# Optimization experiments

Measured on AMD Instinct MI355X. Metric: run time of the kernel, lower is better.

The kernel has to match this reference:

```python
import jax, jax.numpy as jnp
import numpy as np

EMB = 128  # embedding_size hard-coded in source
NW = 8192  # weak samples
NS = 8192  # strong samples
FD = 1024  # encoder input feature dim
QN = 1024  # queue max_size
C = 80     # num classes (COCO-style WSOD)


def setup_inputs() -> dict:
    key = jax.random.key(0)
    ks = jax.random.split(key, 9)
    return {
        "feats_strong": jax.random.normal(ks[0], (NS, FD), jnp.float32),
        "feats_weak": jax.random.normal(ks[1], (NW, FD), jnp.float32),
        "strong_labels": jax.random.randint(ks[2], (NS,), 0, C, jnp.int64),
        "weak_labels": jax.random.randint(ks[3], (NW,), 0, C, jnp.int64),
        "Wq": jax.random.normal(ks[4], (FD, EMB), jnp.float32) * (FD ** -0.5),
        "bq": jax.random.normal(ks[5], (EMB,), jnp.float32) * 0.01,
        "Wk": jax.random.normal(ks[6], (FD, EMB), jnp.float32) * (FD ** -0.5),
        "bk": jax.random.normal(ks[7], (EMB,), jnp.float32) * 0.01,
        "queue": jax.random.normal(ks[8], (QN, EMB), jnp.float32),
    }


def reference(feats_strong, feats_weak, strong_labels, weak_labels, Wq, bq, Wk, bk, queue):
    # Encoders applied to all samples at once (original loops one-by-one).
    q_all = feats_weak @ Wq + bq            # [NW, EMB]
    k_all = feats_strong @ Wk + bk          # [NS, EMB]
    k_all = jax.lax.stop_gradient(k_all)    # k = k.detach() in source

    w, s = weak_labels, strong_labels
    eq_ws = w[:, None] == s[None, :]                      # [NW, NS] weak-vs-strong label match
    cnt = eq_ws.astype(jnp.int32).sum(1)                  # num_strong per weak sample
    valid = cnt > 0                                       # `if weak_label in strong_labels`

    # rank of i among weak indices with the same label (position in torch.where output)
    eq_ww = (w[:, None] == w[None, :]).astype(jnp.int32)
    rank = jnp.tril(eq_ww, -1).sum(1)                     # [NW]
    sel = rank % jnp.maximum(cnt, 1)                      # `% num_strong`

    # occurrence rank of each strong index within its label group
    eq_ss = (s[:, None] == s[None, :]).astype(jnp.int32)
    occ = jnp.tril(eq_ss, -1).sum(1)                      # [NS]

    # index_strong[i] = sel[i]-th strong index whose label == w[i]
    M = eq_ws & (occ[None, :] == sel[:, None])            # [NW, NS]
    idx = jnp.argmax(M, axis=1)                           # [NW]

    q = q_all                                             # [NW, EMB]
    k = k_all[idx]                                        # [NW, EMB]

    l_pos = jnp.sum(q * k, axis=-1, keepdims=True)        # bmm([N,1,E],[N,E,1]) -> [N,1]
    l_neg = q @ queue.reshape(EMB, -1)                    # queue.view(EMB, -1): row-major reshape
    logits = jnp.concatenate([l_pos, l_neg], axis=1)      # [NW, 1+QN]

    # CrossEntropy with target 0 on each valid row, mean over valid rows
    ce = -jax.nn.log_softmax(logits, axis=-1)[:, 0]
    m = valid.astype(logits.dtype)
    loss = jnp.sum(ce * m) / jnp.maximum(m.sum(), 1.0)
    return loss
```

## Files before the change

kernel.cpp:

```cpp
#include <hip/hip_runtime.h>
#include <hip/hip_bf16.h>

#define NW   8192
#define NS   8192
#define FD   1024
#define EMB  128
#define QN   1024
#define NC   80

typedef unsigned short ushort_t;
typedef unsigned int   uint_t;
typedef __attribute__((ext_vector_type(8))) short short8;
typedef __attribute__((ext_vector_type(4))) float f32x4;

#define OFF_Q      0u
#define OFF_K      1048576u
#define OFF_WTQ    2097152u
#define OFF_WTK    2129920u
#define OFF_HIST   2752512u
#define OFF_RANK   2752640u
#define OFF_CNT    2760832u
#define OFF_PART   2760960u
#define OFF_BHS    2785408u
#define OFF_BHW    2787968u
#define OFF_ACC    2790528u
#define OFF_QT     2790532u
#define OFF_TABLE  3000000u

__device__ __forceinline__ ushort_t f2bf(float f) {
    uint_t u = __float_as_uint(f);
    u = (u + 0x7fffu + ((u >> 16) & 1u)) >> 16;
    return (ushort_t)u;
}
__device__ __forceinline__ uint_t pack2(float a, float b) {
    return (uint_t)f2bf(a) | ((uint_t)f2bf(b) << 16);
}

#define GLOAD_LDS16(gp, lp)                                                     \
    __builtin_amdgcn_global_load_lds(                                           \
        (const __attribute__((address_space(1))) void*)(gp),                    \
        (__attribute__((address_space(3))) void*)(lp), 16, 0, 0)

__global__ __launch_bounds__(256) void cvtbh_k(const float* __restrict__ Wq,
                                               const float* __restrict__ Wk,
                                               const float* __restrict__ queue,
                                               const int* __restrict__ s_lab,
                                               const int* __restrict__ w_lab,
                                               ushort_t* __restrict__ Wtq,
                                               ushort_t* __restrict__ Wtk,
                                               ushort_t* __restrict__ Qt,
                                               int* __restrict__ bhs,
                                               int* __restrict__ bhw,
                                               float* __restrict__ accum,
                                               int* __restrict__ counter) {
    int bx = blockIdx.x;
    int t = threadIdx.x;
    if (bx >= 384) {
        __shared__ int h[NC];
        int b2 = bx - 384, z = b2 >> 5, cb = b2 & 31;
        const int* lab = z ? w_lab : s_lab;
        int* bh = z ? bhw : bhs;
        if (t < NC) h[t] = 0;
        __syncthreads();
        atomicAdd(&h[lab[cb * 256 + t]], 1);
        __syncthreads();
        if (t < NC) bh[cb * NC + t] = h[t];
        return;
    }
    __shared__ float tile[32][33];
    int z = bx >> 7, flat = bx & 127;
    if (z == 0 && flat == 0) {
        if (t < 2) accum[t] = 0.0f;
        if (t == 2) *counter = 0;
    }
    const float* in; ushort_t* out; int r0, c0, C;
    if (z < 2) { in = z ? Wk : Wq; out = z ? Wtk : Wtq; C = 128;
                 r0 = (flat >> 2) * 32; c0 = (flat & 3) * 32; }
    else       { in = queue; out = Qt; C = 1024;
                 r0 = (flat & 3) * 32; c0 = (flat >> 2) * 32; }
    int i = t >> 3, j0 = (t & 7) * 4;
    float4 v = *(const float4*)(in + (size_t)(r0 + i) * C + c0 + j0);
    tile[i][j0] = v.x; tile[i][j0 + 1] = v.y; tile[i][j0 + 2] = v.z; tile[i][j0 + 3] = v.w;
    __syncthreads();
    uint2 pk;
    pk.x = pack2(tile[j0][i], tile[j0 + 1][i]);
    pk.y = pack2(tile[j0 + 2][i], tile[j0 + 3][i]);
    size_t oaddr;
    int k0 = r0 + j0, n = c0 + i;
    if (z < 2) {
        oaddr = (size_t)(k0 >> 6) * 8192 + (size_t)((k0 >> 3) & 7) * 1024
              + (size_t)n * 8 + (k0 & 7);
    } else {
        int c = k0 >> 3;
        oaddr = ((size_t)n * 16 + (c ^ (n & 15))) * 8 + (k0 & 7);
    }
    *(uint2*)(out + oaddr) = pk;
}

__global__ __launch_bounds__(256) void enc_mfma_k(const float* __restrict__ A0,
                                                  const float* __restrict__ A1,
                                                  const ushort_t* __restrict__ Wt0,
                                                  const ushort_t* __restrict__ Wt1,
                                                  const float* __restrict__ b0_,
                                                  const float* __restrict__ b1_,
                                                  float* __restrict__ out0,
                                                  float* __restrict__ out1,
                                                  const int* __restrict__ s_lab,
                                                  const int* __restrict__ w_lab,
                                                  const int* __restrict__ bhs,
                                                  const int* __restrict__ bhw,
                                                  int* __restrict__ table,
                                                  int* __restrict__ rank,
                                                  int* __restrict__ hist) {
    __shared__ __align__(16) char smem[73728];

    int bx = blockIdx.x;
    int t = threadIdx.x;

    if (bx < 64) {
        int* ll = (int*)smem;
        int b2 = bx, z = b2 >> 5, cb = b2 & 31;
        const int* lab = z ? w_lab : s_lab;
        const int* bh = z ? bhw : bhs;
        int j = cb * 256 + t;
        int c = lab[j];
        ll[t] = c;
        __syncthreads();
        int r = 0;
        for (int b = 0; b < cb; b++) r += bh[b * NC + c];
        for (int jj = 0; jj < t; jj++) r += (ll[jj] == c) ? 1 : 0;
        if (z) rank[j] = r;
        else   table[c * 8192 + r] = j;
        if (b2 == 0 && t < 128) {
            int h = 0;
            if (t < NC)
                for (int b = 0; b < 32; b++) h += bhs[b * NC + t];
            hist[t] = h;
        }
        return;
    }

    int bxg = bx - 64;
    int which = bxg >> 8;
    int mtile = bxg & 255;
    const float*    A    = which ? A1 : A0;
    const ushort_t* Wt   = which ? Wt1 : Wt0;
    const float*    bias = which ? b1_ : b0_;
    float*          out  = which ? out1 : out0;
    int row0 = mtile * 32;

    int wv = t >> 6, ln = t & 63;
    int wm = wv >> 1, wn = wv & 1;
    int lane15 = ln & 15, kg = ln >> 4;

    int ar0 = wv * 8 + (ln >> 4);
    int ar1 = ar0 + 4;
    const float* gA0 = A + (size_t)(row0 + ar0) * FD + (((ln & 15) ^ (ar0 & 15))) * 4;
    const float* gA1 = A + (size_t)(row0 + ar1) * FD + (((ln & 15) ^ (ar1 & 15))) * 4;
    const ushort_t* gB = Wt + (size_t)wv * 2048 + ln * 8;

    f32x4 acc[4];
#pragma unroll
    for (int nt = 0; nt < 4; nt++) acc[nt] = (f32x4){0.f, 0.f, 0.f, 0.f};

#define STAGE(BUF, KB)                                                           \
    { char* sb = smem + (BUF) * 24576;                                           \
      GLOAD_LDS16(gA0 + (size_t)(KB) * 64, sb + wv * 2048);                      \
      GLOAD_LDS16(gA1 + (size_t)(KB) * 64, sb + wv * 2048 + 1024);               \
      const ushort_t* gb = gB + (size_t)(KB) * 8192;                             \
      char* bb = sb + 8192 + wv * 4096;                                          \
      GLOAD_LDS16(gb,        bb);                                                \
      GLOAD_LDS16(gb + 512,  bb + 1024);                                         \
      GLOAD_LDS16(gb + 1024, bb + 2048);                                         \
      GLOAD_LDS16(gb + 1536, bb + 3072); }

#define K2_ITER(KB, CURB, STB, VMSTR)                                            \
    { asm volatile("s_waitcnt vmcnt(" VMSTR ")" ::: "memory");                   \
      __builtin_amdgcn_s_barrier();                                              \
      __builtin_amdgcn_sched_barrier(0);                                         \
      if ((KB) < 14) STAGE(STB, (KB) + 2)                                        \
      { char* lb = smem + (CURB) * 24576;                                        \
        _Pragma("unroll")                                                        \
        for (int ks = 0; ks < 2; ks++) {                                         \
            int r_l = wm * 16 + lane15;                                          \
            int c0 = ks * 8 + kg * 2;                                            \
            float4 alo = *(const float4*)(lb + ((size_t)r_l * 16 + ((c0)     ^ (r_l & 15))) * 16); \
            float4 ahi = *(const float4*)(lb + ((size_t)r_l * 16 + ((c0 + 1) ^ (r_l & 15))) * 16); \
            uint4 pk;                                                            \
            pk.x = pack2(alo.x, alo.y); pk.y = pack2(alo.z, alo.w);              \
            pk.z = pack2(ahi.x, ahi.y); pk.w = pack2(ahi.z, ahi.w);              \
            short8 af = __builtin_bit_cast(short8, pk);                          \
            int kgg = ks * 4 + kg;                                               \
            _Pragma("unroll")                                                    \
            for (int nt = 0; nt < 4; nt++) {                                     \
                uint4 bv = *(const uint4*)(lb + 8192 +                           \
                            ((size_t)kgg * 128 + wn * 64 + nt * 16 + lane15) * 16); \
                acc[nt] = __builtin_amdgcn_mfma_f32_16x16x32_bf16(               \
                    af, __builtin_bit_cast(short8, bv), acc[nt], 0, 0, 0);       \
            }                                                                    \
        } }                                                                      \
    }

    STAGE(0, 0)
    STAGE(1, 1)
#pragma unroll 1
    for (int kb3 = 0; kb3 < 15; kb3 += 3) {
        K2_ITER(kb3 + 0, 0, 2, "6")
        K2_ITER(kb3 + 1, 1, 0, "6")
        K2_ITER(kb3 + 2, 2, 1, "6")
    }
    K2_ITER(15, 0, 0, "0")
#undef K2_ITER
#undef STAGE

#pragma unroll
    for (int nt = 0; nt < 4; nt++) {
        int col = wn * 64 + nt * 16 + lane15;
        float bv = bias[col];
        int rbase = row0 + wm * 16 + kg * 4;
#pragma unroll
        for (int j = 0; j < 4; j++)
            out[(size_t)(rbase + j) * EMB + col] = acc[nt][j] + bv;
    }
}

__global__ __launch_bounds__(512, 2) void ce_mfma_k(const float* __restrict__ q,
                                                    const float* __restrict__ k,
                                                    const ushort_t* __restrict__ Qt,
                                                    const int* __restrict__ rank,
                                                    const int* __restrict__ table,
                                                    const int* __restrict__ w,
                                                    const int* __restrict__ hist,
                                                    float* __restrict__ part) {
    __shared__ int   idx_lds[32];
    __shared__ float lpos_lds[32];
    __shared__ float mg[8][32][2];
    int t = threadIdx.x;
    int r0 = blockIdx.x * 32;

    if (t < 32) {
        int i = r0 + t;
        int c = w[i];
        int cc = hist[c];
        idx_lds[t] = (cc > 0) ? table[c * 8192 + (rank[i] % cc)] : 0;
    }
    __syncthreads();

    {
        int rr = t >> 4;
        int o = (t & 15) * 8;
        const float4* qa = (const float4*)(q + (size_t)(r0 + rr) * EMB + o);
        const float4* ka = (const float4*)(k + (size_t)idx_lds[rr] * EMB + o);
        float4 a0 = qa[0], b0 = ka[0], a1 = qa[1], b1 = ka[1];
        float s = a0.x * b0.x + a0.y * b0.y + a0.z * b0.z + a0.w * b0.w
                + a1.x * b1.x + a1.y * b1.y + a1.z * b1.z + a1.w * b1.w;
        s += __shfl_xor(s, 1); s += __shfl_xor(s, 2);
        s += __shfl_xor(s, 4); s += __shfl_xor(s, 8);
        if ((t & 15) == 0) lpos_lds[rr] = s;
    }

    int wv = t >> 6, ln = t & 63;
    int wgrp = wv >> 2, wq = wv & 3;
    int lane15 = ln & 15, kg = ln >> 4;

    short8 afrA[4], afrB[4];
#pragma unroll
    for (int ks = 0; ks < 4; ks++) {
        const float4* pA = (const float4*)(q + (size_t)(r0 + lane15) * EMB + ks * 32 + kg * 8);
        const float4* pB = (const float4*)(q + (size_t)(r0 + 16 + lane15) * EMB + ks * 32 + kg * 8);
        float4 a = pA[0], b = pA[1];
        uint4 pk;
        pk.x = pack2(a.x, a.y); pk.y = pack2(a.z, a.w);
        pk.z = pack2(b.x, b.y); pk.w = pack2(b.z, b.w);
        afrA[ks] = __builtin_bit_cast(short8, pk);
        a = pB[0]; b = pB[1];
        pk.x = pack2(a.x, a.y); pk.y = pack2(a.z, a.w);
        pk.z = pack2(b.x, b.y); pk.w = pack2(b.z, b.w);
        afrB[ks] = __builtin_bit_cast(short8, pk);
    }

    f32x4 accA[8], accB[8];
#pragma unroll
    for (int nc = 0; nc < 8; nc++) {
        accA[nc] = (f32x4){0.f, 0.f, 0.f, 0.f};
        accB[nc] = (f32x4){0.f, 0.f, 0.f, 0.f};
    }

#define LOADB(DST, NCI)                                                          \
    { int n_g = ((wgrp * 8 + (NCI)) * 64) + wq * 16 + lane15;                    \
      const ushort_t* bp = Qt + (size_t)n_g * 128;                               \
      _Pragma("unroll")                                                          \
      for (int ks = 0; ks < 4; ks++)                                             \
          DST[ks] = *(const uint4*)(bp + (size_t)(((ks * 4 + kg) ^ lane15)) * 8); }

#define MM2(NC, B)                                                               \
    { _Pragma("unroll")                                                          \
      for (int ks = 0; ks < 4; ks++) {                                           \
          accA[NC] = __builtin_amdgcn_mfma_f32_16x16x32_bf16(                    \
              afrA[ks], __builtin_bit_cast(short8, (B)[ks]), accA[NC], 0, 0, 0); \
          accB[NC] = __builtin_amdgcn_mfma_f32_16x16x32_bf16(                    \
              afrB[ks], __builtin_bit_cast(short8, (B)[ks]), accB[NC], 0, 0, 0); \
      } }

    uint4 b0[4], b1[4];
    LOADB(b0, 0)
    LOADB(b1, 1)  MM2(0, b0)
    LOADB(b0, 2)  MM2(1, b1)
    LOADB(b1, 3)  MM2(2, b0)
    LOADB(b0, 4)  MM2(3, b1)
    LOADB(b1, 5)  MM2(4, b0)
    LOADB(b0, 6)  MM2(5, b1)
    LOADB(b1, 7)  MM2(6, b0)
                  MM2(7, b1)
#undef LOADB
#undef MM2

#pragma unroll
    for (int j = 0; j < 4; j++) {
        float mx = -1e30f;
#pragma unroll
        for (int nc = 0; nc < 8; nc++) mx = fmaxf(mx, accA[nc][j]);
        mx = fmaxf(mx, __shfl_xor(mx, 1));
        mx = fmaxf(mx, __shfl_xor(mx, 2));
        mx = fmaxf(mx, __shfl_xor(mx, 4));
        mx = fmaxf(mx, __shfl_xor(mx, 8));
        float s = 0.f;
#pragma unroll
        for (int nc = 0; nc < 8; nc++) s += __expf(accA[nc][j] - mx);
        s += __shfl_xor(s, 1);
        s += __shfl_xor(s, 2);
        s += __shfl_xor(s, 4);
        s += __shfl_xor(s, 8);
        if (lane15 == 0) {
            mg[wv][kg * 4 + j][0] = mx;
            mg[wv][kg * 4 + j][1] = s;
        }
    }
#pragma unroll
    for (int j = 0; j < 4; j++) {
        float mx = -1e30f;
#pragma unroll
        for (int nc = 0; nc < 8; nc++) mx = fmaxf(mx, accB[nc][j]);
        mx = fmaxf(mx, __shfl_xor(mx, 1));
        mx = fmaxf(mx, __shfl_xor(mx, 2));
        mx = fmaxf(mx, __shfl_xor(mx, 4));
        mx = fmaxf(mx, __shfl_xor(mx, 8));
        float s = 0.f;
#pragma unroll
        for (int nc = 0; nc < 8; nc++) s += __expf(accB[nc][j] - mx);
        s += __shfl_xor(s, 1);
        s += __shfl_xor(s, 2);
        s += __shfl_xor(s, 4);
        s += __shfl_xor(s, 8);
        if (lane15 == 0) {
            mg[wv][16 + kg * 4 + j][0] = mx;
            mg[wv][16 + kg * 4 + j][1] = s;
        }
    }
    __syncthreads();
    if (t < 32) {
        int i = r0 + t;
        float lp = lpos_lds[t];
        float m = lp;
#pragma unroll
        for (int v = 0; v < 8; v++) m = fmaxf(m, mg[v][t][0]);
        float l = __expf(lp - m);
#pragma unroll
        for (int v = 0; v < 8; v++) l += mg[v][t][1] * __expf(mg[v][t][0] - m);
        float ce = -(lp - m - __logf(l));
        float cv = 0.f, cc = 0.f;
        if (hist[w[i]] > 0) { cv = ce; cc = 1.f; }
        cv += __shfl_xor(cv, 1);   cc += __shfl_xor(cc, 1);
        cv += __shfl_xor(cv, 2);   cc += __shfl_xor(cc, 2);
        cv += __shfl_xor(cv, 4);   cc += __shfl_xor(cc, 4);
        cv += __shfl_xor(cv, 8);   cc += __shfl_xor(cc, 8);
        cv += __shfl_xor(cv, 16);  cc += __shfl_xor(cc, 16);
        if (t == 0) {
            float2* pp = (float2*)part;
            pp[blockIdx.x] = make_float2(cv, cc);
        }
    }
}

__global__ __launch_bounds__(256) void fin_k(const float* __restrict__ part,
                                             float* __restrict__ outp) {
    int t = threadIdx.x;
    const float2* pp = (const float2*)part;
    float2 p = pp[t];
    float cv = p.x, cc = p.y;
    cv += __shfl_xor(cv, 1);   cc += __shfl_xor(cc, 1);
    cv += __shfl_xor(cv, 2);   cc += __shfl_xor(cc, 2);
    cv += __shfl_xor(cv, 4);   cc += __shfl_xor(cc, 4);
    cv += __shfl_xor(cv, 8);   cc += __shfl_xor(cc, 8);
    cv += __shfl_xor(cv, 16);  cc += __shfl_xor(cc, 16);
    cv += __shfl_xor(cv, 32);  cc += __shfl_xor(cc, 32);
    __shared__ float sv[4], sc[4];
    if ((t & 63) == 0) { sv[t >> 6] = cv; sc[t >> 6] = cc; }
    __syncthreads();
    if (t == 0) {
        float s = sv[0] + sv[1] + sv[2] + sv[3];
        float c = sc[0] + sc[1] + sc[2] + sc[3];
        outp[0] = s / fmaxf(c, 1.0f);
    }
}

extern "C" void kernel_launch(void* const* d_in, const int* in_sizes, int n_in,
                              void* d_out, int out_size, void* d_ws, size_t ws_size,
                              hipStream_t stream) {
    const float* feats_strong = (const float*)d_in[0];
    const float* feats_weak   = (const float*)d_in[1];
    const int*   s_lab        = (const int*)d_in[2];
    const int*   w_lab        = (const int*)d_in[3];
    const float* Wq           = (const float*)d_in[4];
    const float* bq           = (const float*)d_in[5];
    const float* Wk           = (const float*)d_in[6];
    const float* bk           = (const float*)d_in[7];
    const float* queue        = (const float*)d_in[8];

    float*    wsf = (float*)d_ws;
    int*      wsi = (int*)d_ws;

    float*    q_g   = wsf + OFF_Q;
    float*    k_g   = wsf + OFF_K;
    int*      table = wsi + OFF_TABLE;
    ushort_t* Wtq   = (ushort_t*)(wsi + OFF_WTQ);
    ushort_t* Wtk   = (ushort_t*)(wsi + OFF_WTK);
    int*      hist  = wsi + OFF_HIST;
    int*      rank  = wsi + OFF_RANK;
    int*      cnt   = wsi + OFF_CNT;
    int*      bhs   = wsi + OFF_BHS;
    int*      bhw   = wsi + OFF_BHW;
    float*    accum = wsf + OFF_ACC;
    float*    part  = wsf + OFF_PART;
    ushort_t* Qt    = (ushort_t*)(wsi + OFF_QT);

    cvtbh_k<<<448, 256, 0, stream>>>(Wq, Wk, queue, s_lab, w_lab,
                                     Wtq, Wtk, Qt, bhs, bhw, accum, cnt);
    enc_mfma_k<<<576, 256, 0, stream>>>(feats_weak, feats_strong, Wtq, Wtk, bq, bk, q_g, k_g,
                                        s_lab, w_lab, bhs, bhw, table, rank, hist);
    ce_mfma_k<<<256, 512, 0, stream>>>(q_g, k_g, Qt, rank, table, w_lab, hist, part);
    fin_k<<<1, 256, 0, stream>>>(part, (float*)d_out);
}
```

Baseline: 142.7 us.

## Read encoder weights from global, prefetch queue tiles early, fuse final reduction

The encoder kernel stops staging the bf16 weight tiles in LDS and reads them directly from global memory (L2-resident). This cuts shared memory from 72KB to 24KB and adds a launch bound of 4 blocks per SM to raise occupancy. The CE kernel issues its first queue-tile loads before the label/l_pos phase and reorders loads after MMAs. The separate finalize kernel is replaced by a last-block-done atomic counter inside the CE kernel, which removes one launch. The risks are extra L2/global traffic for the weight reads, and correctness that depends on the counter being zeroed every call.

```diff
diff --git a/kernel.cpp b/kernel.cpp
--- a/kernel.cpp
+++ b/kernel.cpp
@@ -97,22 +97,22 @@
     *(uint2*)(out + oaddr) = pk;
 }
 
-__global__ __launch_bounds__(256) void enc_mfma_k(const float* __restrict__ A0,
-                                                  const float* __restrict__ A1,
-                                                  const ushort_t* __restrict__ Wt0,
-                                                  const ushort_t* __restrict__ Wt1,
-                                                  const float* __restrict__ b0_,
-                                                  const float* __restrict__ b1_,
-                                                  float* __restrict__ out0,
-                                                  float* __restrict__ out1,
-                                                  const int* __restrict__ s_lab,
-                                                  const int* __restrict__ w_lab,
-                                                  const int* __restrict__ bhs,
-                                                  const int* __restrict__ bhw,
-                                                  int* __restrict__ table,
-                                                  int* __restrict__ rank,
-                                                  int* __restrict__ hist) {
-    __shared__ __align__(16) char smem[73728];
+__global__ __launch_bounds__(256, 4) void enc_mfma_k(const float* __restrict__ A0,
+                                                     const float* __restrict__ A1,
+                                                     const ushort_t* __restrict__ Wt0,
+                                                     const ushort_t* __restrict__ Wt1,
+                                                     const float* __restrict__ b0_,
+                                                     const float* __restrict__ b1_,
+                                                     float* __restrict__ out0,
+                                                     float* __restrict__ out1,
+                                                     const int* __restrict__ s_lab,
+                                                     const int* __restrict__ w_lab,
+                                                     const int* __restrict__ bhs,
+                                                     const int* __restrict__ bhw,
+                                                     int* __restrict__ table,
+                                                     int* __restrict__ rank,
+                                                     int* __restrict__ hist) {
+    __shared__ __align__(16) char smem[24576];
 
     int bx = blockIdx.x;
     int t = threadIdx.x;
@@ -157,29 +157,23 @@
     int ar1 = ar0 + 4;
     const float* gA0 = A + (size_t)(row0 + ar0) * FD + (((ln & 15) ^ (ar0 & 15))) * 4;
     const float* gA1 = A + (size_t)(row0 + ar1) * FD + (((ln & 15) ^ (ar1 & 15))) * 4;
-    const ushort_t* gB = Wt + (size_t)wv * 2048 + ln * 8;
 
     f32x4 acc[4];
 #pragma unroll
     for (int nt = 0; nt < 4; nt++) acc[nt] = (f32x4){0.f, 0.f, 0.f, 0.f};
 
 #define STAGE(BUF, KB)                                                           \
-    { char* sb = smem + (BUF) * 24576;                                           \
+    { char* sb = smem + (BUF) * 8192;                                            \
       GLOAD_LDS16(gA0 + (size_t)(KB) * 64, sb + wv * 2048);                      \
-      GLOAD_LDS16(gA1 + (size_t)(KB) * 64, sb + wv * 2048 + 1024);               \
-      const ushort_t* gb = gB + (size_t)(KB) * 8192;                             \
-      char* bb = sb + 8192 + wv * 4096;                                          \
-      GLOAD_LDS16(gb,        bb);                                                \
-      GLOAD_LDS16(gb + 512,  bb + 1024);                                         \
-      GLOAD_LDS16(gb + 1024, bb + 2048);                                         \
-      GLOAD_LDS16(gb + 1536, bb + 3072); }
+      GLOAD_LDS16(gA1 + (size_t)(KB) * 64, sb + wv * 2048 + 1024); }
 
 #define K2_ITER(KB, CURB, STB, VMSTR)                                            \
     { asm volatile("s_waitcnt vmcnt(" VMSTR ")" ::: "memory");                   \
       __builtin_amdgcn_s_barrier();                                              \
       __builtin_amdgcn_sched_barrier(0);                                         \
       if ((KB) < 14) STAGE(STB, (KB) + 2)                                        \
-      { char* lb = smem + (CURB) * 24576;                                        \
+      { char* lb = smem + (CURB) * 8192;                                         \
+        const ushort_t* wtb = Wt + (size_t)(KB) * 8192;                          \
         _Pragma("unroll")                                                        \
         for (int ks = 0; ks < 2; ks++) {                                         \
             int r_l = wm * 16 + lane15;                                          \
@@ -193,8 +187,8 @@
             int kgg = ks * 4 + kg;                                               \
             _Pragma("unroll")                                                    \
             for (int nt = 0; nt < 4; nt++) {                                     \
-                uint4 bv = *(const uint4*)(lb + 8192 +                           \
-                            ((size_t)kgg * 128 + wn * 64 + nt * 16 + lane15) * 16); \
+                uint4 bv = *(const uint4*)(wtb +                                 \
+                            ((size_t)kgg * 128 + wn * 64 + nt * 16 + lane15) * 8); \
                 acc[nt] = __builtin_amdgcn_mfma_f32_16x16x32_bf16(               \
                     af, __builtin_bit_cast(short8, bv), acc[nt], 0, 0, 0);       \
             }                                                                    \
@@ -205,9 +199,9 @@
     STAGE(1, 1)
 #pragma unroll 1
     for (int kb3 = 0; kb3 < 15; kb3 += 3) {
-        K2_ITER(kb3 + 0, 0, 2, "6")
-        K2_ITER(kb3 + 1, 1, 0, "6")
-        K2_ITER(kb3 + 2, 2, 1, "6")
+        K2_ITER(kb3 + 0, 0, 2, "2")
+        K2_ITER(kb3 + 1, 1, 0, "2")
+        K2_ITER(kb3 + 2, 2, 1, "2")
     }
     K2_ITER(15, 0, 0, "0")
 #undef K2_ITER
@@ -231,12 +225,30 @@
                                                     const int* __restrict__ table,
                                                     const int* __restrict__ w,
                                                     const int* __restrict__ hist,
-                                                    float* __restrict__ part) {
+                                                    float* __restrict__ part,
+                                                    int* __restrict__ counter,
+                                                    float* __restrict__ outp) {
     __shared__ int   idx_lds[32];
     __shared__ float lpos_lds[32];
     __shared__ float mg[8][32][2];
+    __shared__ int   amlast;
     int t = threadIdx.x;
     int r0 = blockIdx.x * 32;
+
+    int wv = t >> 6, ln = t & 63;
+    int wgrp = wv >> 2, wq = wv & 3;
+    int lane15 = ln & 15, kg = ln >> 4;
+
+#define LOADB(DST, NCI)                                                          \
+    { int n_g = ((wgrp * 8 + (NCI)) * 64) + wq * 16 + lane15;                    \
+      const ushort_t* bp = Qt + (size_t)n_g * 128;                               \
+      _Pragma("unroll")                                                          \
+      for (int ks = 0; ks < 4; ks++)                                             \
+          DST[ks] = *(const uint4*)(bp + (size_t)(((ks * 4 + kg) ^ lane15)) * 8); }
+
+    uint4 b0[4], b1[4];
+    LOADB(b0, 0)
+    LOADB(b1, 1)
 
     if (t < 32) {
         int i = r0 + t;
@@ -251,17 +263,13 @@
         int o = (t & 15) * 8;
         const float4* qa = (const float4*)(q + (size_t)(r0 + rr) * EMB + o);
         const float4* ka = (const float4*)(k + (size_t)idx_lds[rr] * EMB + o);
-        float4 a0 = qa[0], b0 = ka[0], a1 = qa[1], b1 = ka[1];
-        float s = a0.x * b0.x + a0.y * b0.y + a0.z * b0.z + a0.w * b0.w
-                + a1.x * b1.x + a1.y * b1.y + a1.z * b1.z + a1.w * b1.w;
+        float4 a0 = qa[0], bb0 = ka[0], a1 = qa[1], bb1 = ka[1];
+        float s = a0.x * bb0.x + a0.y * bb0.y + a0.z * bb0.z + a0.w * bb0.w
+                + a1.x * bb1.x + a1.y * bb1.y + a1.z * bb1.z + a1.w * bb1.w;
         s += __shfl_xor(s, 1); s += __shfl_xor(s, 2);
         s += __shfl_xor(s, 4); s += __shfl_xor(s, 8);
         if ((t & 15) == 0) lpos_lds[rr] = s;
     }
-
-    int wv = t >> 6, ln = t & 63;
-    int wgrp = wv >> 2, wq = wv & 3;
-    int lane15 = ln & 15, kg = ln >> 4;
 
     short8 afrA[4], afrB[4];
 #pragma unroll
@@ -286,13 +294,6 @@
         accB[nc] = (f32x4){0.f, 0.f, 0.f, 0.f};
     }
 
-#define LOADB(DST, NCI)                                                          \
-    { int n_g = ((wgrp * 8 + (NCI)) * 64) + wq * 16 + lane15;                    \
-      const ushort_t* bp = Qt + (size_t)n_g * 128;                               \
-      _Pragma("unroll")                                                          \
-      for (int ks = 0; ks < 4; ks++)                                             \
-          DST[ks] = *(const uint4*)(bp + (size_t)(((ks * 4 + kg) ^ lane15)) * 8); }
-
 #define MM2(NC, B)                                                               \
     { _Pragma("unroll")                                                          \
       for (int ks = 0; ks < 4; ks++) {                                           \
@@ -302,16 +303,14 @@
               afrB[ks], __builtin_bit_cast(short8, (B)[ks]), accB[NC], 0, 0, 0); \
       } }
 
-    uint4 b0[4], b1[4];
-    LOADB(b0, 0)
-    LOADB(b1, 1)  MM2(0, b0)
-    LOADB(b0, 2)  MM2(1, b1)
-    LOADB(b1, 3)  MM2(2, b0)
-    LOADB(b0, 4)  MM2(3, b1)
-    LOADB(b1, 5)  MM2(4, b0)
-    LOADB(b0, 6)  MM2(5, b1)
-    LOADB(b1, 7)  MM2(6, b0)
-                  MM2(7, b1)
+    MM2(0, b0)  LOADB(b0, 2)
+    MM2(1, b1)  LOADB(b1, 3)
+    MM2(2, b0)  LOADB(b0, 4)
+    MM2(3, b1)  LOADB(b1, 5)
+    MM2(4, b0)  LOADB(b0, 6)
+    MM2(5, b1)  LOADB(b1, 7)
+    MM2(6, b0)
+    MM2(7, b1)
 #undef LOADB
 #undef MM2
 
@@ -378,29 +377,30 @@
         if (t == 0) {
             float2* pp = (float2*)part;
             pp[blockIdx.x] = make_float2(cv, cc);
+            __threadfence();
+            amlast = (atomicAdd(counter, 1) == 255) ? 1 : 0;
         }
     }
-}
-
-__global__ __launch_bounds__(256) void fin_k(const float* __restrict__ part,
-                                             float* __restrict__ outp) {
-    int t = threadIdx.x;
-    const float2* pp = (const float2*)part;
-    float2 p = pp[t];
-    float cv = p.x, cc = p.y;
-    cv += __shfl_xor(cv, 1);   cc += __shfl_xor(cc, 1);
-    cv += __shfl_xor(cv, 2);   cc += __shfl_xor(cc, 2);
-    cv += __shfl_xor(cv, 4);   cc += __shfl_xor(cc, 4);
-    cv += __shfl_xor(cv, 8);   cc += __shfl_xor(cc, 8);
-    cv += __shfl_xor(cv, 16);  cc += __shfl_xor(cc, 16);
-    cv += __shfl_xor(cv, 32);  cc += __shfl_xor(cc, 32);
-    __shared__ float sv[4], sc[4];
-    if ((t & 63) == 0) { sv[t >> 6] = cv; sc[t >> 6] = cc; }
     __syncthreads();
-    if (t == 0) {
-        float s = sv[0] + sv[1] + sv[2] + sv[3];
-        float c = sc[0] + sc[1] + sc[2] + sc[3];
-        outp[0] = s / fmaxf(c, 1.0f);
+    if (amlast) {
+        __threadfence();
+        const float2* pp = (const float2*)part;
+        float cv = 0.f, cc = 0.f;
+        if (t < 256) { float2 p = pp[t]; cv = p.x; cc = p.y; }
+        cv += __shfl_xor(cv, 1);   cc += __shfl_xor(cc, 1);
+        cv += __shfl_xor(cv, 2);   cc += __shfl_xor(cc, 2);
+        cv += __shfl_xor(cv, 4);   cc += __shfl_xor(cc, 4);
+        cv += __shfl_xor(cv, 8);   cc += __shfl_xor(cc, 8);
+        cv += __shfl_xor(cv, 16);  cc += __shfl_xor(cc, 16);
+        cv += __shfl_xor(cv, 32);  cc += __shfl_xor(cc, 32);
+        __shared__ float sv[4], sc[4];
+        if (t < 256 && ln == 0) { sv[wv] = cv; sc[wv] = cc; }
+        __syncthreads();
+        if (t == 0) {
+            float s = sv[0] + sv[1] + sv[2] + sv[3];
+            float c = sc[0] + sc[1] + sc[2] + sc[3];
+            outp[0] = s / fmaxf(c, 1.0f);
+        }
     }
 }
 
@@ -438,6 +438,6 @@
                                      Wtq, Wtk, Qt, bhs, bhw, accum, cnt);
     enc_mfma_k<<<576, 256, 0, stream>>>(feats_weak, feats_strong, Wtq, Wtk, bq, bk, q_g, k_g,
                                         s_lab, w_lab, bhs, bhw, table, rank, hist);
-    ce_mfma_k<<<256, 512, 0, stream>>>(q_g, k_g, Qt, rank, table, w_lab, hist, part);
-    fin_k<<<1, 256, 0, stream>>>(part, (float*)d_out);
-}
+    ce_mfma_k<<<256, 512, 0, stream>>>(q_g, k_g, Qt, rank, table, w_lab, hist,
+                                       part, cnt, (float*)d_out);
+}
```

After: 147.4 us. +3.3%, slower.
